# Performance work log

Hardware: AMD Instinct MI355X
Metric: run time of the kernel (lower is better)

The kernel has to match this reference:

```python
import jax, jax.numpy as jnp
import numpy as np

VOCAB, EMBED, HIDDEN = 32000, 512, 1024
B, T = 2, 2048
LN_EPS = 1e-5


def setup_inputs() -> dict:
    key = jax.random.key(0)
    ks = jax.random.split(key, 12)

    def xavier(k, fan_in, fan_out):
        lim = float(np.sqrt(6.0 / (fan_in + fan_out)))
        return jax.random.uniform(k, (fan_in, fan_out), jnp.float32, -lim, lim)

    return {
        "tokens": jax.random.randint(ks[0], (B, T), 0, VOCAB),
        "E": xavier(ks[1], VOCAB, EMBED),                    # embedding table
        "Wc": xavier(ks[2], EMBED, HIDDEN),                  # fc_current (stored [in,out])
        "bc": jnp.full((HIDDEN,), 0.01, jnp.float32),
        "Wh": xavier(ks[3], EMBED, HIDDEN),                  # fc_context
        "bh": jnp.full((HIDDEN,), 0.01, jnp.float32),
        "Wm": xavier(ks[4], 2 * HIDDEN, HIDDEN),             # fc_merge
        "bm": jnp.full((HIDDEN,), 0.01, jnp.float32),
        "Wo": xavier(ks[5], HIDDEN, VOCAB),                  # fc_out
        "bo": jnp.full((VOCAB,), 0.01, jnp.float32),
        "ln_w": jnp.ones((HIDDEN,), jnp.float32),
        "ln_b": jnp.zeros((HIDDEN,), jnp.float32),
    }


def reference(tokens, E, Wc, bc, Wh, bh, Wm, bm, Wo, bo, ln_w, ln_b):
    emb = E[tokens]  # [B, T, D]
    # history mean at step t = mean(emb[:, :t]); at t==0 the module uses current embed
    csum = jnp.cumsum(emb, axis=1)
    counts = jnp.arange(1, T, dtype=emb.dtype)[None, :, None]
    hist_mean = jnp.concatenate([emb[:, :1], csum[:, :-1] / counts], axis=1)  # [B,T,D]

    cur_enc = jax.nn.relu(jnp.einsum("btd,dh->bth", emb, Wc) + bc)
    hist_enc = jax.nn.relu(jnp.einsum("btd,dh->bth", hist_mean, Wh) + bh)
    merged = jnp.concatenate([cur_enc, hist_enc], axis=-1)  # [B,T,2H]
    merged = jax.nn.relu(jnp.einsum("btk,kh->bth", merged, Wm) + bm)

    mu = jnp.mean(merged, axis=-1, keepdims=True)
    var = jnp.mean(jnp.square(merged - mu), axis=-1, keepdims=True)
    normed = (merged - mu) * jax.lax.rsqrt(var + LN_EPS) * ln_w + ln_b

    logits = (jnp.einsum("bth,hv->btv", normed, Wo) + bo) / 10.0  # [B,T,V]
    return logits
```

## Files before the change

kernel.cpp:

```cpp
#include <hip/hip_runtime.h>
#include <hip/hip_bf16.h>
#include <stdint.h>
#include <stdio.h>

#define T_SEQ  2048
#define BATCH  2
#define NROWS  4096
#define EMBED  512
#define HIDDEN 1024
#define VOCAB  32000
#define NCHUNK 32
#define CHLEN  64

typedef __bf16 bf16x8 __attribute__((ext_vector_type(8)));
typedef float  f32x4  __attribute__((ext_vector_type(4)));

__device__ __forceinline__ float b2f(unsigned short h) {
  union { unsigned int u; float f; } v; v.u = ((unsigned int)h) << 16; return v.f;
}
__device__ __forceinline__ unsigned short f2b(float f) {
  union { float f; unsigned int u; } v; v.f = f;
  unsigned int u = v.u;
  u += 0x7fffu + ((u >> 16) & 1u);
  return (unsigned short)(u >> 16);
}

__global__ void gather_sum_kernel(const int* __restrict__ tokens,
                                  const float* __restrict__ E,
                                  unsigned short* __restrict__ emb,
                                  float* __restrict__ csum) {
  const int bc = blockIdx.x;
  const int d  = threadIdx.x;
  __shared__ int tok[CHLEN];
  if (d < CHLEN) tok[d] = tokens[bc * CHLEN + d];
  __syncthreads();
  float s = 0.f;
  unsigned short* eo = emb + ((size_t)bc * CHLEN) * EMBED + d;
  #pragma unroll 4
  for (int i = 0; i < CHLEN; ++i) {
    const float v = E[(size_t)tok[i] * EMBED + d];
    const unsigned short h = f2b(v);
    eo[(size_t)i * EMBED] = h;
    s += b2f(h);
  }
  csum[(size_t)bc * EMBED + d] = s;
}

__global__ void scan_excl_kernel(float* __restrict__ csum) {
  const int b = blockIdx.x;
  const int d = threadIdx.x;
  float run = 0.f;
  for (int c = 0; c < NCHUNK; ++c) {
    const size_t idx = ((size_t)b * NCHUNK + c) * EMBED + d;
    const float v = csum[idx];
    csum[idx] = run;
    run += v;
  }
}

__global__ void scan_emit_kernel(const unsigned short* __restrict__ emb,
                                 const float* __restrict__ csum,
                                 unsigned short* __restrict__ hist) {
  const int bc = blockIdx.x;
  const int c  = bc & (NCHUNK - 1);
  const int d  = threadIdx.x;
  const unsigned short* e = emb  + ((size_t)bc * CHLEN) * EMBED + d;
  unsigned short*       h = hist + ((size_t)bc * CHLEN) * EMBED + d;
  float sum = csum[(size_t)bc * EMBED + d];
  #pragma unroll 8
  for (int i = 0; i < CHLEN; ++i) {
    const int t = c * CHLEN + i;
    h[(size_t)i * EMBED] = (t == 0) ? e[0] : f2b(sum / (float)t);
    sum += b2f(e[(size_t)i * EMBED]);
  }
}

__global__ __launch_bounds__(256) void transpose_all_kernel(
    const float* __restrict__ Wc, const float* __restrict__ Wh,
    const float* __restrict__ Wm, const float* __restrict__ Wo,
    unsigned short* __restrict__ WcT, unsigned short* __restrict__ WhT,
    unsigned short* __restrict__ WmT, unsigned short* __restrict__ WoT) {
  const int id = blockIdx.x;
  const float* in; unsigned short* out; int R, C, t;
  if (id < 128)      { in = Wc; out = WcT; R = 512;  C = 1024;  t = id; }
  else if (id < 256) { in = Wh; out = WhT; R = 512;  C = 1024;  t = id - 128; }
  else if (id < 768) { in = Wm; out = WmT; R = 2048; C = 1024;  t = id - 256; }
  else               { in = Wo; out = WoT; R = 1024; C = 32000; t = id - 768; }
  const int tilesX = C >> 6;
  const int r0 = (t / tilesX) << 6, c0 = (t % tilesX) << 6;

  __shared__ float tile[64][65];
  const int tid = threadIdx.x;
  #pragma unroll
  for (int p = 0; p < 4; ++p) {
    const int u = tid + p * 256;
    const int row = u >> 4, cq = (u & 15) << 2;
    const float4 v = *(const float4*)&in[(size_t)(r0 + row) * C + c0 + cq];
    tile[row][cq + 0] = v.x; tile[row][cq + 1] = v.y;
    tile[row][cq + 2] = v.z; tile[row][cq + 3] = v.w;
  }
  __syncthreads();
  #pragma unroll
  for (int p = 0; p < 4; ++p) {
    const int u = tid + p * 256;
    const int oc = u >> 4, org = (u & 15) << 2;
    ushort4 o;
    o.x = f2b(tile[org + 0][oc]); o.y = f2b(tile[org + 1][oc]);
    o.z = f2b(tile[org + 2][oc]); o.w = f2b(tile[org + 3][oc]);
    *(ushort4*)&out[(size_t)(c0 + oc) * R + r0 + org] = o;
  }
}

__device__ __forceinline__ void async16(unsigned short* lds, const unsigned short* g) {
  __builtin_amdgcn_global_load_lds(
      (const __attribute__((address_space(1))) void*)g,
      (__attribute__((address_space(3))) void*)lds, 16, 0, 0);
}

#define BM 128
#define BN 128
#define BK 32

template<int MODE>
__global__ __launch_bounds__(256) void gemm_bt_kernel(
    const unsigned short* __restrict__ A,
    const unsigned short* __restrict__ BT,
    const float* __restrict__ bias,
    void* __restrict__ out, int M, int N, int K, int ldOut, int colOff,
    const unsigned short* __restrict__ A2,
    const unsigned short* __restrict__ BT2,
    const float* __restrict__ bias2, int colOff2) {
  __shared__ unsigned short As[BM * BK];
  __shared__ unsigned short Bs[BN * BK];

  const unsigned short* Ap = A;
  const unsigned short* Bp = BT;
  const float*          bp = bias;
  int                   co = colOff;
  if (blockIdx.z) { Ap = A2; Bp = BT2; bp = bias2; co = colOff2; }

  int wg = blockIdx.x;
  {
    const int nwg = gridDim.x;
    const int xcd = wg & 7, loc = wg >> 3;
    const int q = nwg >> 3, r = nwg & 7;
    wg = (xcd < r ? xcd * (q + 1) : r * (q + 1) + (xcd - r) * q) + loc;
  }
  const int nmb = M / BM;
  const int mb  = wg % nmb;
  const int nb  = wg / nmb;
  const int m0  = mb * BM;
  const int n0  = nb * BN;

  const int tid  = threadIdx.x;
  const int wave = tid >> 6;
  const int lane = tid & 63;
  const int wm = (wave & 1) * 64;
  const int wn = (wave >> 1) * 64;

  const int srow = (wave << 5) + (lane >> 2);
  const int scol = (lane & 3) << 3;
  const unsigned short* aSrc = Ap + (size_t)(m0 + srow) * K + scol;
  const unsigned short* bSrc = Bp + (size_t)(n0 + srow) * K + scol;
  unsigned short* aDst = As + (wave << 5) * BK;
  unsigned short* bDst = Bs + (wave << 5) * BK;

  f32x4 acc[4][4];
  #pragma unroll
  for (int i = 0; i < 4; ++i)
    #pragma unroll
    for (int j = 0; j < 4; ++j)
      acc[i][j] = (f32x4){0.f, 0.f, 0.f, 0.f};

  const int q = lane >> 4;
  const int r = lane & 15;

  for (int k0 = 0; k0 < K; k0 += BK) {
    __syncthreads();
    async16(aDst,           aSrc);
    async16(aDst + 16 * BK, aSrc + 16 * (size_t)K);
    async16(bDst,           bSrc);
    async16(bDst + 16 * BK, bSrc + 16 * (size_t)K);
    aSrc += BK; bSrc += BK;
    __syncthreads();

    bf16x8 af[4], bfr[4];
    #pragma unroll
    for (int mi = 0; mi < 4; ++mi)
      af[mi] = *(const bf16x8*)&As[(wm + mi * 16 + r) * BK + (q << 3)];
    #pragma unroll
    for (int ni = 0; ni < 4; ++ni)
      bfr[ni] = *(const bf16x8*)&Bs[(wn + ni * 16 + r) * BK + (q << 3)];
    #pragma unroll
    for (int mi = 0; mi < 4; ++mi)
      #pragma unroll
      for (int ni = 0; ni < 4; ++ni)
        acc[mi][ni] = __builtin_amdgcn_mfma_f32_16x16x32_bf16(
            af[mi], bfr[ni], acc[mi][ni], 0, 0, 0);
  }

  #pragma unroll
  for (int ni = 0; ni < 4; ++ni) {
    const int col = n0 + wn + ni * 16 + r;
    const float bv = bp[col];
    #pragma unroll
    for (int mi = 0; mi < 4; ++mi) {
      #pragma unroll
      for (int e = 0; e < 4; ++e) {
        const int row = m0 + wm + mi * 16 + (q << 2) + e;
        float v = fmaxf(acc[mi][ni][e] + bv, 0.f);
        const size_t idx = (size_t)row * ldOut + co + col;
        if (MODE == 0) ((unsigned short*)out)[idx] = f2b(v);
        else           ((float*)out)[idx] = v;
      }
    }
  }
}


#define BAR() do {                            \
    asm volatile("" ::: "memory");            \
    __builtin_amdgcn_sched_barrier(0);        \
    __builtin_amdgcn_s_barrier();             \
    __builtin_amdgcn_sched_barrier(0);        \
    asm volatile("" ::: "memory");            \
  } while (0)

__global__ __launch_bounds__(512, 2) void gemm256_out_kernel(
    const unsigned short* __restrict__ A,
    const unsigned short* __restrict__ BT,
    const float* __restrict__ bias,
    float* __restrict__ out, int M, int N, int K, int ldOut) {
  __shared__ unsigned short lds[2][2][2][8192];

  int wg = blockIdx.x;
  {
    const int nwg = gridDim.x;
    const int xcd = wg & 7, loc = wg >> 3;
    const int q8 = nwg >> 3, r8 = nwg & 7;
    wg = (xcd < r8 ? xcd * (q8 + 1) : r8 * (q8 + 1) + (xcd - r8) * q8) + loc;
  }
  const int nmb = M >> 8;
  const int mb = wg % nmb, nb = wg / nmb;
  const int m0 = mb << 8, n0 = nb << 8;

  const int tid  = threadIdx.x;
  const int wave = tid >> 6, lane = tid & 63;
  const int wr = wave >> 2, wc = wave & 3;
  const int q = lane >> 4, r = lane & 15, rr = lane & 7;

  const int srow = (wave << 4) + (lane >> 3);
  const int scol = ((lane & 7) ^ (lane >> 3)) << 3;
  const unsigned short* aB = A  + (size_t)(m0 + srow) * K + scol;
  const unsigned short* bB = BT + (size_t)(n0 + srow) * K + scol;

  const int NTt = K >> 6;

  auto stage = [&](int matB, int h, int tb, int kt) {
    unsigned short* d = &lds[tb][matB][h][wave << 10];
    const unsigned short* s =
        (matB ? bB : aB) + (size_t)h * 128 * K + ((size_t)kt << 6);
    async16(d, s);
    async16(d + 512, s + ((size_t)K << 3));
  };

  auto ldA = [&](int tb, int mi, int ks) {
    return *(const bf16x8*)&lds[tb][0][wr]
        [(mi * 16 + r) * 64 + ((((ks << 2) | q) ^ rr) << 3)];
  };
  auto ldB = [&](int tb, int ni, int ks) {
    return *(const bf16x8*)&lds[tb][1][wc >> 1]
        [(((wc & 1) << 6) + ni * 16 + r) * 64 + ((((ks << 2) | q) ^ rr) << 3)];
  };

  f32x4 acc[8][4];
  #pragma unroll
  for (int i = 0; i < 8; ++i)
    #pragma unroll
    for (int j = 0; j < 4; ++j)
      acc[i][j] = (f32x4){0.f, 0.f, 0.f, 0.f};

  bf16x8 afr[8][2], bfr[2][2];

  stage(0, 0, 0, 0); stage(0, 1, 0, 0); stage(1, 0, 0, 0); stage(1, 1, 0, 0);
  if (NTt > 1) {
    stage(0, 0, 1, 1); stage(0, 1, 1, 1); stage(1, 0, 1, 1);
    asm volatile("s_waitcnt vmcnt(6)" ::: "memory");
  } else {
    asm volatile("s_waitcnt vmcnt(0)" ::: "memory");
  }
  BAR();

#define TILE(U, BU) do {                                                       \
    const int u_ = (U);                                                        \
                            \
    _Pragma("unroll")                                                          \
    for (int mi = 0; mi < 4; ++mi) {                                           \
      afr[mi][0] = ldA(BU, mi, 0); afr[mi][1] = ldA(BU, mi, 1);                \
    }                                                                          \
    _Pragma("unroll")                                                          \
    for (int nj = 0; nj < 2; ++nj) {                                           \
      bfr[nj][0] = ldB(BU, nj, 0); bfr[nj][1] = ldB(BU, nj, 1);                \
    }                                                                          \
    if (u_ + 1 < NTt) stage(1, 1, 1 - (BU), u_ + 1);                           \
    __builtin_amdgcn_s_setprio(1);                                             \
    _Pragma("unroll")                                                          \
    for (int mi = 0; mi < 4; ++mi)                                             \
      _Pragma("unroll")                                                        \
      for (int nj = 0; nj < 2; ++nj) {                                         \
        acc[mi][nj] = __builtin_amdgcn_mfma_f32_16x16x32_bf16(                 \
            afr[mi][0], bfr[nj][0], acc[mi][nj], 0, 0, 0);                     \
        acc[mi][nj] = __builtin_amdgcn_mfma_f32_16x16x32_bf16(                 \
            afr[mi][1], bfr[nj][1], acc[mi][nj], 0, 0, 0);                     \
      }                                                                        \
    __builtin_amdgcn_s_setprio(0);                                             \
    BAR();                                                                     \
                                 \
    _Pragma("unroll")                                                          \
    for (int mi = 4; mi < 8; ++mi) {                                           \
      afr[mi][0] = ldA(BU, mi, 0); afr[mi][1] = ldA(BU, mi, 1);                \
    }                                                                          \
    __builtin_amdgcn_s_setprio(1);                                             \
    _Pragma("unroll")                                                          \
    for (int mi = 4; mi < 8; ++mi)                                             \
      _Pragma("unroll")                                                        \
      for (int nj = 0; nj < 2; ++nj) {                                         \
        acc[mi][nj] = __builtin_amdgcn_mfma_f32_16x16x32_bf16(                 \
            afr[mi][0], bfr[nj][0], acc[mi][nj], 0, 0, 0);                     \
        acc[mi][nj] = __builtin_amdgcn_mfma_f32_16x16x32_bf16(                 \
            afr[mi][1], bfr[nj][1], acc[mi][nj], 0, 0, 0);                     \
      }                                                                        \
    __builtin_amdgcn_s_setprio(0);                                             \
    BAR();                                                                     \
                            \
    _Pragma("unroll")                                                          \
    for (int nj = 0; nj < 2; ++nj) {                                           \
      bfr[nj][0] = ldB(BU, 2 + nj, 0); bfr[nj][1] = ldB(BU, 2 + nj, 1);        \
    }                                                                          \
    if (u_ + 2 < NTt) stage(0, 0, BU, u_ + 2);                                 \
    __builtin_amdgcn_s_setprio(1);                                             \
    _Pragma("unroll")                                                          \
    for (int mi = 0; mi < 4; ++mi)                                             \
      _Pragma("unroll")                                                        \
      for (int nj = 0; nj < 2; ++nj) {                                         \
        acc[mi][2 + nj] = __builtin_amdgcn_mfma_f32_16x16x32_bf16(             \
            afr[mi][0], bfr[nj][0], acc[mi][2 + nj], 0, 0, 0);                 \
        acc[mi][2 + nj] = __builtin_amdgcn_mfma_f32_16x16x32_bf16(             \
            afr[mi][1], bfr[nj][1], acc[mi][2 + nj], 0, 0, 0);                 \
      }                                                                        \
    __builtin_amdgcn_s_setprio(0);                                             \
    BAR();                                                                     \
                   \
    if (u_ + 2 < NTt) { stage(0, 1, BU, u_ + 2); stage(1, 0, BU, u_ + 2); }    \
    __builtin_amdgcn_s_setprio(1);                                             \
    _Pragma("unroll")                                                          \
    for (int mi = 4; mi < 8; ++mi)                                             \
      _Pragma("unroll")                                                        \
      for (int nj = 0; nj < 2; ++nj) {                                         \
        acc[mi][2 + nj] = __builtin_amdgcn_mfma_f32_16x16x32_bf16(             \
            afr[mi][0], bfr[nj][0], acc[mi][2 + nj], 0, 0, 0);                 \
        acc[mi][2 + nj] = __builtin_amdgcn_mfma_f32_16x16x32_bf16(             \
            afr[mi][1], bfr[nj][1], acc[mi][2 + nj], 0, 0, 0);                 \
      }                                                                        \
    __builtin_amdgcn_s_setprio(0);                                             \
    if (u_ + 2 < NTt) asm volatile("s_waitcnt vmcnt(6)" ::: "memory");         \
    else              asm volatile("s_waitcnt vmcnt(0)" ::: "memory");         \
    BAR();                                                                     \
  } while (0)

  for (int u = 0; u < NTt; u += 2) {
    TILE(u, 0);
    TILE(u + 1, 1);
  }
#undef TILE

  float* scratch = (float*)&lds[0][0][0][0];
  #pragma unroll
  for (int p = 0; p < 2; ++p) {
    if (wr == p) {
      #pragma unroll
      for (int ni = 0; ni < 4; ++ni) {
        const int col = (wc << 6) + ni * 16 + r;
        const float bv = bias[n0 + col];
        #pragma unroll
        for (int mi = 0; mi < 8; ++mi) {
          #pragma unroll
          for (int e = 0; e < 4; ++e) {
            const int row = mi * 16 + (q << 2) + e;
            const int cs  = col ^ (((row >> 2) & 1) << 4);
            scratch[row * 256 + cs] = (acc[mi][ni][e] + bv) * 0.1f;
          }
        }
      }
    }
    __syncthreads();
    #pragma unroll
    for (int rowi = 0; rowi < 16; ++rowi) {
      const int row = (wave << 4) + rowi;
      const int cb  = (lane << 2) ^ (((row >> 2) & 1) << 4);
      const f32x4 v4 = *(const f32x4*)&scratch[row * 256 + cb];
      *(f32x4*)&out[(size_t)(m0 + (p << 7) + row) * ldOut + n0 + (lane << 2)] = v4;
    }
    __syncthreads();
  }
}

__global__ void ln_kernel(const float* __restrict__ merged,
                          const float* __restrict__ lnw,
                          const float* __restrict__ lnb,
                          unsigned short* __restrict__ normed) {
  const int row = blockIdx.x;
  const float4 v = ((const float4*)(merged + (size_t)row * HIDDEN))[threadIdx.x];
  float s  = v.x + v.y + v.z + v.w;
  float ss = v.x * v.x + v.y * v.y + v.z * v.z + v.w * v.w;
  #pragma unroll
  for (int off = 32; off > 0; off >>= 1) {
    s  += __shfl_down(s, off, 64);
    ss += __shfl_down(ss, off, 64);
  }
  __shared__ float red[8];
  const int wvi = threadIdx.x >> 6;
  if ((threadIdx.x & 63) == 0) { red[wvi] = s; red[4 + wvi] = ss; }
  __syncthreads();
  s  = red[0] + red[1] + red[2] + red[3];
  ss = red[4] + red[5] + red[6] + red[7];
  const float mu  = s * (1.0f / HIDDEN);
  const float var = ss * (1.0f / HIDDEN) - mu * mu;
  const float rs  = rsqrtf(var + 1e-5f);
  const float4 w4 = ((const float4*)lnw)[threadIdx.x];
  const float4 b4 = ((const float4*)lnb)[threadIdx.x];
  ushort4 o;
  o.x = f2b((v.x - mu) * rs * w4.x + b4.x);
  o.y = f2b((v.y - mu) * rs * w4.y + b4.y);
  o.z = f2b((v.z - mu) * rs * w4.z + b4.z);
  o.w = f2b((v.w - mu) * rs * w4.w + b4.w);
  ((ushort4*)(normed + (size_t)row * HIDDEN))[threadIdx.x] = o;
}

extern "C" void kernel_launch(void* const* d_in, const int* in_sizes, int n_in,
                              void* d_out, int out_size, void* d_ws, size_t ws_size,
                              hipStream_t stream) {
  const int*   tokens = (const int*)d_in[0];
  const float* E      = (const float*)d_in[1];
  const float* Wc     = (const float*)d_in[2];
  const float* bc     = (const float*)d_in[3];
  const float* Wh     = (const float*)d_in[4];
  const float* bh     = (const float*)d_in[5];
  const float* Wm     = (const float*)d_in[6];
  const float* bm     = (const float*)d_in[7];
  const float* Wo     = (const float*)d_in[8];
  const float* bo     = (const float*)d_in[9];
  const float* lnw    = (const float*)d_in[10];
  const float* lnb    = (const float*)d_in[11];

  char* p = (char*)d_ws;
  unsigned short* WcT  = (unsigned short*)p; p += (size_t)HIDDEN * EMBED * 2;
  unsigned short* WhT  = (unsigned short*)p; p += (size_t)HIDDEN * EMBED * 2;
  unsigned short* WmT  = (unsigned short*)p; p += (size_t)HIDDEN * (2 * HIDDEN) * 2;
  unsigned short* WoT  = (unsigned short*)p; p += (size_t)VOCAB * HIDDEN * 2;
  unsigned short* emb  = (unsigned short*)p; p += (size_t)NROWS * EMBED * 2;
  unsigned short* hist = (unsigned short*)p; p += (size_t)NROWS * EMBED * 2;
  unsigned short* cat  = (unsigned short*)p; p += (size_t)NROWS * (2 * HIDDEN) * 2;
  float*          mrg  = (float*)p;          p += (size_t)NROWS * HIDDEN * 4;
  unsigned short* nrm  = (unsigned short*)p; p += (size_t)NROWS * HIDDEN * 2;
  float*          csum = (float*)p;          p += (size_t)BATCH * NCHUNK * EMBED * 4;
  if ((size_t)(p - (char*)d_ws) > ws_size)
    fprintf(stderr, "WS TOO SMALL: need %zu have %zu\n", (size_t)(p - (char*)d_ws), ws_size);

  transpose_all_kernel<<<8768, 256, 0, stream>>>(Wc, Wh, Wm, Wo, WcT, WhT, WmT, WoT);

  gather_sum_kernel<<<BATCH * NCHUNK, EMBED, 0, stream>>>(tokens, E, emb, csum);
  scan_excl_kernel<<<BATCH, EMBED, 0, stream>>>(csum);
  scan_emit_kernel<<<BATCH * NCHUNK, EMBED, 0, stream>>>(emb, csum, hist);

  const int nwgEnc = (NROWS / BM) * (HIDDEN / BN);

  gemm_bt_kernel<0><<<dim3(nwgEnc, 1, 2), 256, 0, stream>>>(
      emb, WcT, bc, cat, NROWS, HIDDEN, EMBED, 2 * HIDDEN, 0,
      hist, WhT, bh, HIDDEN);
  gemm_bt_kernel<1><<<dim3(nwgEnc, 1, 1), 256, 0, stream>>>(
      cat, WmT, bm, mrg, NROWS, HIDDEN, 2 * HIDDEN, HIDDEN, 0,
      nullptr, nullptr, nullptr, 0);
  ln_kernel<<<NROWS, 256, 0, stream>>>(mrg, lnw, lnb, nrm);

  const int nwgOut = (NROWS / 256) * (VOCAB / 256);
  gemm256_out_kernel<<<dim3(nwgOut), 512, 0, stream>>>(
      nrm, WoT, bo, (float*)d_out, NROWS, VOCAB, HIDDEN, VOCAB);
}
```

Baseline: 986.2 us.

## Shrink output GEMM to 128x128 tiles and parallelize history scan chunks

Replaces the 256x256, 512-thread output-projection GEMM with a 128x128, 256-thread kernel using K-steps of 32, a simpler double-buffered pipeline, and a new LDS swizzle and epilogue. The scan prep moves to 128 chunks of 16 tokens, and the exclusive scan is split across blocks over the embedding dimension with an LDS prefetch. The goal is more workgroups and occupancy, plus more parallel, shorter scan stages. The smaller tile lowers data reuse per block and doubles the number of K iterations and barriers, which may hurt the dominant vocab GEMM.

```diff
diff --git a/kernel.cpp b/kernel.cpp
--- a/kernel.cpp
+++ b/kernel.cpp
@@ -9,8 +9,8 @@
 #define EMBED  512
 #define HIDDEN 1024
 #define VOCAB  32000
-#define NCHUNK 32
-#define CHLEN  64
+#define NCHUNK 128
+#define CHLEN  16
 
 typedef __bf16 bf16x8 __attribute__((ext_vector_type(8)));
 typedef float  f32x4  __attribute__((ext_vector_type(4)));
@@ -47,13 +47,16 @@
 }
 
 __global__ void scan_excl_kernel(float* __restrict__ csum) {
-  const int b = blockIdx.x;
-  const int d = threadIdx.x;
+  const int b  = blockIdx.x;
+  const int d0 = blockIdx.y << 7;
+  const int t  = threadIdx.x;
+  __shared__ float s[NCHUNK][128];
+  for (int c = 0; c < NCHUNK; ++c)
+    s[c][t] = csum[((size_t)b * NCHUNK + c) * EMBED + d0 + t];
   float run = 0.f;
   for (int c = 0; c < NCHUNK; ++c) {
-    const size_t idx = ((size_t)b * NCHUNK + c) * EMBED + d;
-    const float v = csum[idx];
-    csum[idx] = run;
+    const float v = s[c][t];
+    csum[((size_t)b * NCHUNK + c) * EMBED + d0 + t] = run;
     run += v;
   }
 }
@@ -226,12 +229,12 @@
     asm volatile("" ::: "memory");            \
   } while (0)
 
-__global__ __launch_bounds__(512, 2) void gemm256_out_kernel(
+__global__ __launch_bounds__(256, 4) void gemm_out_kernel(
     const unsigned short* __restrict__ A,
     const unsigned short* __restrict__ BT,
     const float* __restrict__ bias,
     float* __restrict__ out, int M, int N, int K, int ldOut) {
-  __shared__ unsigned short lds[2][2][2][8192];
+  __shared__ unsigned short lds[2][2][4096];
 
   int wg = blockIdx.x;
   {
@@ -240,166 +243,111 @@
     const int q8 = nwg >> 3, r8 = nwg & 7;
     wg = (xcd < r8 ? xcd * (q8 + 1) : r8 * (q8 + 1) + (xcd - r8) * q8) + loc;
   }
-  const int nmb = M >> 8;
+  const int nmb = M >> 7;
   const int mb = wg % nmb, nb = wg / nmb;
-  const int m0 = mb << 8, n0 = nb << 8;
+  const int m0 = mb << 7, n0 = nb << 7;
 
   const int tid  = threadIdx.x;
   const int wave = tid >> 6, lane = tid & 63;
-  const int wr = wave >> 2, wc = wave & 3;
-  const int q = lane >> 4, r = lane & 15, rr = lane & 7;
-
-  const int srow = (wave << 4) + (lane >> 3);
-  const int scol = ((lane & 7) ^ (lane >> 3)) << 3;
+  const int wm = (wave & 1) << 6, wn = (wave >> 1) << 6;
+  const int q = lane >> 4, r = lane & 15;
+
+  const int srow = (wave << 5) + (lane >> 2);
+  const int scol = ((lane & 3) ^ ((lane >> 2) & 3)) << 3;
   const unsigned short* aB = A  + (size_t)(m0 + srow) * K + scol;
   const unsigned short* bB = BT + (size_t)(n0 + srow) * K + scol;
 
-  const int NTt = K >> 6;
-
-  auto stage = [&](int matB, int h, int tb, int kt) {
-    unsigned short* d = &lds[tb][matB][h][wave << 10];
-    const unsigned short* s =
-        (matB ? bB : aB) + (size_t)h * 128 * K + ((size_t)kt << 6);
+  const int NTt = K >> 5;
+
+  auto stage = [&](int matB, int tb, int kt) {
+    unsigned short* d = &lds[tb][matB][wave << 10];
+    const unsigned short* s = (matB ? bB : aB) + ((size_t)kt << 5);
     async16(d, s);
-    async16(d + 512, s + ((size_t)K << 3));
+    async16(d + 512, s + ((size_t)K << 4));
   };
 
-  auto ldA = [&](int tb, int mi, int ks) {
-    return *(const bf16x8*)&lds[tb][0][wr]
-        [(mi * 16 + r) * 64 + ((((ks << 2) | q) ^ rr) << 3)];
+  auto ldA = [&](int tb, int mi) {
+    const int row = wm + mi * 16 + r;
+    return *(const bf16x8*)&lds[tb][0][(row << 5) + ((q ^ (r & 3)) << 3)];
   };
-  auto ldB = [&](int tb, int ni, int ks) {
-    return *(const bf16x8*)&lds[tb][1][wc >> 1]
-        [(((wc & 1) << 6) + ni * 16 + r) * 64 + ((((ks << 2) | q) ^ rr) << 3)];
+  auto ldB = [&](int tb, int nj) {
+    const int row = wn + nj * 16 + r;
+    return *(const bf16x8*)&lds[tb][1][(row << 5) + ((q ^ (r & 3)) << 3)];
   };
 
-  f32x4 acc[8][4];
-  #pragma unroll
-  for (int i = 0; i < 8; ++i)
+  f32x4 acc[4][4];
+  #pragma unroll
+  for (int i = 0; i < 4; ++i)
     #pragma unroll
     for (int j = 0; j < 4; ++j)
       acc[i][j] = (f32x4){0.f, 0.f, 0.f, 0.f};
 
-  bf16x8 afr[8][2], bfr[2][2];
-
-  stage(0, 0, 0, 0); stage(0, 1, 0, 0); stage(1, 0, 0, 0); stage(1, 1, 0, 0);
+  stage(0, 0, 0); stage(1, 0, 0);
   if (NTt > 1) {
-    stage(0, 0, 1, 1); stage(0, 1, 1, 1); stage(1, 0, 1, 1);
-    asm volatile("s_waitcnt vmcnt(6)" ::: "memory");
+    stage(0, 1, 1); stage(1, 1, 1);
+    asm volatile("s_waitcnt vmcnt(4)" ::: "memory");
   } else {
     asm volatile("s_waitcnt vmcnt(0)" ::: "memory");
   }
   BAR();
 
-#define TILE(U, BU) do {                                                       \
-    const int u_ = (U);                                                        \
-                            \
-    _Pragma("unroll")                                                          \
-    for (int mi = 0; mi < 4; ++mi) {                                           \
-      afr[mi][0] = ldA(BU, mi, 0); afr[mi][1] = ldA(BU, mi, 1);                \
-    }                                                                          \
-    _Pragma("unroll")                                                          \
-    for (int nj = 0; nj < 2; ++nj) {                                           \
-      bfr[nj][0] = ldB(BU, nj, 0); bfr[nj][1] = ldB(BU, nj, 1);                \
-    }                                                                          \
-    if (u_ + 1 < NTt) stage(1, 1, 1 - (BU), u_ + 1);                           \
-    __builtin_amdgcn_s_setprio(1);                                             \
-    _Pragma("unroll")                                                          \
-    for (int mi = 0; mi < 4; ++mi)                                             \
-      _Pragma("unroll")                                                        \
-      for (int nj = 0; nj < 2; ++nj) {                                         \
-        acc[mi][nj] = __builtin_amdgcn_mfma_f32_16x16x32_bf16(                 \
-            afr[mi][0], bfr[nj][0], acc[mi][nj], 0, 0, 0);                     \
-        acc[mi][nj] = __builtin_amdgcn_mfma_f32_16x16x32_bf16(                 \
-            afr[mi][1], bfr[nj][1], acc[mi][nj], 0, 0, 0);                     \
-      }                                                                        \
-    __builtin_amdgcn_s_setprio(0);                                             \
-    BAR();                                                                     \
-                                 \
-    _Pragma("unroll")                                                          \
-    for (int mi = 4; mi < 8; ++mi) {                                           \
-      afr[mi][0] = ldA(BU, mi, 0); afr[mi][1] = ldA(BU, mi, 1);                \
-    }                                                                          \
-    __builtin_amdgcn_s_setprio(1);                                             \
-    _Pragma("unroll")                                                          \
-    for (int mi = 4; mi < 8; ++mi)                                             \
-      _Pragma("unroll")                                                        \
-      for (int nj = 0; nj < 2; ++nj) {                                         \
-        acc[mi][nj] = __builtin_amdgcn_mfma_f32_16x16x32_bf16(                 \
-            afr[mi][0], bfr[nj][0], acc[mi][nj], 0, 0, 0);                     \
-        acc[mi][nj] = __builtin_amdgcn_mfma_f32_16x16x32_bf16(                 \
-            afr[mi][1], bfr[nj][1], acc[mi][nj], 0, 0, 0);                     \
-      }                                                                        \
-    __builtin_amdgcn_s_setprio(0);                                             \
-    BAR();                                                                     \
-                            \
-    _Pragma("unroll")                                                          \
-    for (int nj = 0; nj < 2; ++nj) {                                           \
-      bfr[nj][0] = ldB(BU, 2 + nj, 0); bfr[nj][1] = ldB(BU, 2 + nj, 1);        \
-    }                                                                          \
-    if (u_ + 2 < NTt) stage(0, 0, BU, u_ + 2);                                 \
-    __builtin_amdgcn_s_setprio(1);                                             \
-    _Pragma("unroll")                                                          \
-    for (int mi = 0; mi < 4; ++mi)                                             \
-      _Pragma("unroll")                                                        \
-      for (int nj = 0; nj < 2; ++nj) {                                         \
-        acc[mi][2 + nj] = __builtin_amdgcn_mfma_f32_16x16x32_bf16(             \
-            afr[mi][0], bfr[nj][0], acc[mi][2 + nj], 0, 0, 0);                 \
-        acc[mi][2 + nj] = __builtin_amdgcn_mfma_f32_16x16x32_bf16(             \
-            afr[mi][1], bfr[nj][1], acc[mi][2 + nj], 0, 0, 0);                 \
-      }                                                                        \
-    __builtin_amdgcn_s_setprio(0);                                             \
-    BAR();                                                                     \
-                   \
-    if (u_ + 2 < NTt) { stage(0, 1, BU, u_ + 2); stage(1, 0, BU, u_ + 2); }    \
-    __builtin_amdgcn_s_setprio(1);                                             \
-    _Pragma("unroll")                                                          \
-    for (int mi = 4; mi < 8; ++mi)                                             \
-      _Pragma("unroll")                                                        \
-      for (int nj = 0; nj < 2; ++nj) {                                         \
-        acc[mi][2 + nj] = __builtin_amdgcn_mfma_f32_16x16x32_bf16(             \
-            afr[mi][0], bfr[nj][0], acc[mi][2 + nj], 0, 0, 0);                 \
-        acc[mi][2 + nj] = __builtin_amdgcn_mfma_f32_16x16x32_bf16(             \
-            afr[mi][1], bfr[nj][1], acc[mi][2 + nj], 0, 0, 0);                 \
-      }                                                                        \
-    __builtin_amdgcn_s_setprio(0);                                             \
-    if (u_ + 2 < NTt) asm volatile("s_waitcnt vmcnt(6)" ::: "memory");         \
-    else              asm volatile("s_waitcnt vmcnt(0)" ::: "memory");         \
-    BAR();                                                                     \
-  } while (0)
-
-  for (int u = 0; u < NTt; u += 2) {
-    TILE(u, 0);
-    TILE(u + 1, 1);
-  }
-#undef TILE
-
-  float* scratch = (float*)&lds[0][0][0][0];
-  #pragma unroll
-  for (int p = 0; p < 2; ++p) {
-    if (wr == p) {
+  for (int u = 0; u < NTt; ++u) {
+    const int bu = u & 1;
+    bf16x8 af[4], bf[4];
+    #pragma unroll
+    for (int mi = 0; mi < 4; ++mi) af[mi] = ldA(bu, mi);
+    #pragma unroll
+    for (int nj = 0; nj < 4; ++nj) bf[nj] = ldB(bu, nj);
+    __builtin_amdgcn_s_setprio(1);
+    #pragma unroll
+    for (int mi = 0; mi < 2; ++mi)
       #pragma unroll
-      for (int ni = 0; ni < 4; ++ni) {
-        const int col = (wc << 6) + ni * 16 + r;
+      for (int nj = 0; nj < 4; ++nj)
+        acc[mi][nj] = __builtin_amdgcn_mfma_f32_16x16x32_bf16(
+            af[mi], bf[nj], acc[mi][nj], 0, 0, 0);
+    __builtin_amdgcn_s_setprio(0);
+    BAR();
+    if (u + 2 < NTt) { stage(0, bu, u + 2); stage(1, bu, u + 2); }
+    __builtin_amdgcn_s_setprio(1);
+    #pragma unroll
+    for (int mi = 2; mi < 4; ++mi)
+      #pragma unroll
+      for (int nj = 0; nj < 4; ++nj)
+        acc[mi][nj] = __builtin_amdgcn_mfma_f32_16x16x32_bf16(
+            af[mi], bf[nj], acc[mi][nj], 0, 0, 0);
+    __builtin_amdgcn_s_setprio(0);
+    if (u + 2 < NTt) asm volatile("s_waitcnt vmcnt(4)" ::: "memory");
+    else             asm volatile("s_waitcnt vmcnt(0)" ::: "memory");
+    BAR();
+  }
+
+  float* scratch = (float*)&lds[0][0][0];
+  const int wmi = wave & 1;
+  #pragma unroll
+  for (int g = 0; g < 2; ++g) {
+    if (wmi == g) {
+      #pragma unroll
+      for (int nj = 0; nj < 4; ++nj) {
+        const int col = wn + nj * 16 + r;
         const float bv = bias[n0 + col];
         #pragma unroll
-        for (int mi = 0; mi < 8; ++mi) {
+        for (int mi = 0; mi < 4; ++mi) {
           #pragma unroll
           for (int e = 0; e < 4; ++e) {
             const int row = mi * 16 + (q << 2) + e;
-            const int cs  = col ^ (((row >> 2) & 1) << 4);
-            scratch[row * 256 + cs] = (acc[mi][ni][e] + bv) * 0.1f;
+            scratch[row * 128 + (col ^ (q << 4))] = (acc[mi][nj][e] + bv) * 0.1f;
           }
         }
       }
     }
     __syncthreads();
     #pragma unroll
-    for (int rowi = 0; rowi < 16; ++rowi) {
-      const int row = (wave << 4) + rowi;
-      const int cb  = (lane << 2) ^ (((row >> 2) & 1) << 4);
-      const f32x4 v4 = *(const f32x4*)&scratch[row * 256 + cb];
-      *(f32x4*)&out[(size_t)(m0 + (p << 7) + row) * ldOut + n0 + (lane << 2)] = v4;
+    for (int i = 0; i < 8; ++i) {
+      const int row = (wave << 4) + (i << 1) + (lane >> 5);
+      const int cb  = (lane & 31) << 2;
+      const f32x4 v4 =
+          *(const f32x4*)&scratch[row * 128 + (cb ^ (((row >> 2) & 3) << 4))];
+      *(f32x4*)&out[(size_t)(m0 + (g << 6) + row) * ldOut + n0 + cb] = v4;
     }
     __syncthreads();
   }
@@ -470,7 +418,7 @@
   transpose_all_kernel<<<8768, 256, 0, stream>>>(Wc, Wh, Wm, Wo, WcT, WhT, WmT, WoT);
 
   gather_sum_kernel<<<BATCH * NCHUNK, EMBED, 0, stream>>>(tokens, E, emb, csum);
-  scan_excl_kernel<<<BATCH, EMBED, 0, stream>>>(csum);
+  scan_excl_kernel<<<dim3(BATCH, EMBED / 128), 128, 0, stream>>>(csum);
   scan_emit_kernel<<<BATCH * NCHUNK, EMBED, 0, stream>>>(emb, csum, hist);
 
   const int nwgEnc = (NROWS / BM) * (HIDDEN / BN);
@@ -483,7 +431,7 @@
       nullptr, nullptr, nullptr, 0);
   ln_kernel<<<NROWS, 256, 0, stream>>>(mrg, lnw, lnb, nrm);
 
-  const int nwgOut = (NROWS / 256) * (VOCAB / 256);
-  gemm256_out_kernel<<<dim3(nwgOut), 512, 0, stream>>>(
+  const int nwgOut = (NROWS / 128) * (VOCAB / 128);
+  gemm_out_kernel<<<dim3(nwgOut), 256, 0, stream>>>(
       nrm, WoT, bo, (float*)d_out, NROWS, VOCAB, HIDDEN, VOCAB);
 }
```

Result: slower. 1.077 ms (+9.3%).
